# Performance work log

Hardware: AMD Instinct MI355X
Metric: run time of the kernel (lower is better)

Reference implementation:

```python
import jax, jax.numpy as jnp
import numpy as np

VOCAB = 1_000_000
EMBED_DIM = 128
BATCH = 16_384
NOISE_COUNT = 16


def setup_inputs() -> dict:
    key = jax.random.key(0)
    k1, k2, k3, k4, k5, k6 = jax.random.split(key, 6)
    embed = jax.random.uniform(k1, (EMBED_DIM, VOCAB), jnp.float32, -1.0, 1.0)
    bias = jax.random.uniform(k2, (VOCAB, 1), jnp.float32, -1.0, 1.0)
    u = jax.random.uniform(k3, (VOCAB,), jnp.float32, 1e-3, 1.0)
    freq = u / u.sum()  # normalized unigram^0.75 noise distribution
    targets = jax.random.randint(k4, (BATCH,), 0, VOCAB)
    contexts = jax.random.randint(k5, (BATCH,), 0, VOCAB)
    noises = jax.random.randint(k6, (BATCH * NOISE_COUNT,), 0, VOCAB)
    return {"embed": embed, "bias": bias, "freq": freq,
            "targets": targets, "contexts": contexts, "noises": noises,
            "noise_count": NOISE_COUNT}


def reference(embed, bias, freq, targets, contexts, noises, noise_count):
    # embed: (E, V); bias: (V, 1); freq: (V,)
    E = embed.shape[0]
    B = targets.shape[0]
    re = 10.0
    q = embed[:, targets]                      # (E, B) target embeddings
    r = embed[:, contexts]                     # (E, B) context embeddings
    b = bias[targets, 0][None, :]              # (1, B)
    s = ((r * q).sum(0)[None, :] + b) / E      # (1, B) scaled score
    # positive term: log(sigmoid(s - log(k * p(target))))
    pos = jax.nn.log_sigmoid(s - jnp.log(noise_count * freq[targets]))
    loss = pos.sum()
    # noise term: log(1 - sigmoid(tile(s,k) - log(k * p(noise)))) = log_sigmoid(-x)
    s_tiled = jnp.tile(s, (1, noise_count))    # (1, B*k) == torch.cat((s,)*k, dim=1)
    noise_loss = jax.nn.log_sigmoid(-(s_tiled - jnp.log(noise_count * freq[noises]))).sum()
    total_loss = -(loss + noise_loss) / B
    penalty = re * ((q * q).sum() + (r * r).sum()) / (E * B)
    return total_loss + penalty
```

## Files before the change

kernel.cpp:

```cpp
#include <hip/hip_runtime.h>
#include <math.h>


#define NB 2048

__device__ __forceinline__ float log_sigmoid_f(float x) {
    return fminf(x, 0.0f) - log1pf(expf(-fabsf(x)));
}

__device__ __forceinline__ int task_col(int i, const int* __restrict__ targets,
                                        const int* __restrict__ contexts) {
    const int pair = i >> 1;
    return (i & 1) ? contexts[pair] : targets[pair];
}

__global__ __launch_bounds__(256) void hist_kernel(
    const int* __restrict__ targets, const int* __restrict__ contexts,
    int* __restrict__ counts, int T2, int sh)
{
    const int i = blockIdx.x * 256 + threadIdx.x;
    if (i < T2) atomicAdd(&counts[task_col(i, targets, contexts) >> sh], 1);
}

__global__ __launch_bounds__(1024) void scan_kernel(
    const int* __restrict__ counts, int* __restrict__ cursors, int nb)
{
    __shared__ int a[NB], b[NB];
    for (int i = threadIdx.x; i < NB; i += 1024) a[i] = (i < nb) ? counts[i] : 0;
    __syncthreads();
    int* src = a; int* dst = b;
    for (int off = 1; off < NB; off <<= 1) {
        for (int i = threadIdx.x; i < NB; i += 1024)
            dst[i] = src[i] + (i >= off ? src[i - off] : 0);
        __syncthreads();
        int* t = src; src = dst; dst = t;
    }
    for (int i = threadIdx.x; i < NB; i += 1024)
        if (i < nb) cursors[i] = src[i] - counts[i];
}

__global__ __launch_bounds__(256) void scatter_kernel(
    const int* __restrict__ targets, const int* __restrict__ contexts,
    int* __restrict__ cursors, int* __restrict__ sorted,
    int* __restrict__ invperm, int T2, int sh)
{
    const int i = blockIdx.x * 256 + threadIdx.x;
    if (i < T2) {
        const int col = task_col(i, targets, contexts);
        const int pos = atomicAdd(&cursors[col >> sh], 1);
        sorted[pos] = i;
        invperm[i]  = pos;
    }
}

__global__ __launch_bounds__(256) void gather_kernel(
    const float* __restrict__ embed,
    const int* __restrict__ targets, const int* __restrict__ contexts,
    const int* __restrict__ sorted, float* __restrict__ dense,
    int V, int T2)
{
    const int p = threadIdx.x & 15;
    const int g = threadIdx.x >> 4;
    const int pos = blockIdx.x * 16 + p;
    if (pos >= T2) return;
    const int col = task_col(sorted[pos], targets, contexts);
    const int e0 = g * 8;
    const float* src = embed + col;
    float v[8];
    #pragma unroll
    for (int k = 0; k < 8; ++k) v[k] = src[(size_t)(e0 + k) * V];
    float4* dst = (float4*)(dense + (size_t)pos * 128 + e0);
    dst[0] = make_float4(v[0], v[1], v[2], v[3]);
    dst[1] = make_float4(v[4], v[5], v[6], v[7]);
}

__global__ __launch_bounds__(256) void compute_kernel(
    const float* __restrict__ dense, const int* __restrict__ invperm,
    const float* __restrict__ bias, const float* __restrict__ freq,
    const int* __restrict__ targets, const int* __restrict__ noises,
    float* __restrict__ partials, int B, int NC)
{
    __shared__ float sh_dot[16][17];
    __shared__ float sh_sq [16][17];
    __shared__ float sh_s  [16];
    __shared__ float sh_wred[4];

    const int p = threadIdx.x & 15;
    const int g = threadIdx.x >> 4;
    const int j = blockIdx.x * 16 + p;
    const bool valid = (j < B);

    float contrib = 0.0f;
    float dot = 0.0f, sq = 0.0f;
    float lg0 = 0.0f; bool has0 = false;
    float bval = 0.0f, lgt = 0.0f;

    if (valid) {
        if (g < NC) {
            const int n = noises[j + (size_t)g * B];
            lg0 = logf((float)NC * freq[n]);
            has0 = true;
        }
        if (g == 0) {
            const int t = targets[j];
            bval = bias[t];
            lgt  = logf((float)NC * freq[t]);
        }
        const int e0 = g * 8;
        const float4* qv = (const float4*)(dense + (size_t)invperm[2 * j]     * 128 + e0);
        const float4* rv = (const float4*)(dense + (size_t)invperm[2 * j + 1] * 128 + e0);
        const float4 q0 = qv[0], q1 = qv[1];
        const float4 r0 = rv[0], r1 = rv[1];
        dot = fmaf(q0.x, r0.x, fmaf(q0.y, r0.y, fmaf(q0.z, r0.z, fmaf(q0.w, r0.w,
              fmaf(q1.x, r1.x, fmaf(q1.y, r1.y, fmaf(q1.z, r1.z, q1.w * r1.w)))))));
        sq  = fmaf(q0.x, q0.x, fmaf(q0.y, q0.y, fmaf(q0.z, q0.z, fmaf(q0.w, q0.w,
              fmaf(q1.x, q1.x, fmaf(q1.y, q1.y, fmaf(q1.z, q1.z, fmaf(q1.w, q1.w,
              fmaf(r0.x, r0.x, fmaf(r0.y, r0.y, fmaf(r0.z, r0.z, fmaf(r0.w, r0.w,
              fmaf(r1.x, r1.x, fmaf(r1.y, r1.y, fmaf(r1.z, r1.z, r1.w * r1.w)))))))))))))));
    }
    sh_dot[p][g] = dot;
    sh_sq [p][g] = sq;
    __syncthreads();

    if (threadIdx.x < 16) {
        float d = 0.0f, s2 = 0.0f;
        #pragma unroll
        for (int gg = 0; gg < 16; ++gg) {
            d  += sh_dot[threadIdx.x][gg];
            s2 += sh_sq [threadIdx.x][gg];
        }
        float sval = 0.0f;
        if (valid) {
            sval = (d + bval) / 128.0f;
            const float pos = log_sigmoid_f(sval - lgt);
            contrib += -pos / (float)B + 10.0f * s2 / (128.0f * (float)B);
        }
        sh_s[threadIdx.x] = sval;
    }
    __syncthreads();

    if (valid) {
        const float sval = sh_s[p];
        float nacc = 0.0f;
        if (has0) nacc = log_sigmoid_f(-(sval - lg0));
        for (int k = g + 16; k < NC; k += 16) {
            const int n = noises[j + (size_t)k * B];
            nacc += log_sigmoid_f(-(sval - logf((float)NC * freq[n])));
        }
        contrib += -nacc / (float)B;
    }

    #pragma unroll
    for (int off = 32; off > 0; off >>= 1)
        contrib += __shfl_xor(contrib, off, 64);
    const int wave = threadIdx.x >> 6;
    if ((threadIdx.x & 63) == 0) sh_wred[wave] = contrib;
    __syncthreads();
    if (threadIdx.x == 0)
        partials[blockIdx.x] = sh_wred[0] + sh_wred[1] + sh_wred[2] + sh_wred[3];
}

__global__ __launch_bounds__(256) void reduce_partials_kernel(
    const float* __restrict__ parts, int n, float* __restrict__ out)
{
    __shared__ double sh[256];
    double a = 0.0;
    for (int i = threadIdx.x; i < n; i += 256) a += (double)parts[i];
    sh[threadIdx.x] = a;
    __syncthreads();
    for (int s = 128; s > 0; s >>= 1) {
        if (threadIdx.x < s) sh[threadIdx.x] += sh[threadIdx.x + s];
        __syncthreads();
    }
    if (threadIdx.x == 0) out[0] = (float)sh[0];
}

__global__ __launch_bounds__(256) void nce_fallback(
    const float* __restrict__ embed, const float* __restrict__ bias,
    const float* __restrict__ freq, const int* __restrict__ targets,
    const int* __restrict__ contexts, const int* __restrict__ noises,
    float* __restrict__ block_partials, int V, int E, int B, int NC)
{
    __shared__ float sh_dot[16][17];
    __shared__ float sh_sq [16][17];
    __shared__ float sh_s  [16];
    __shared__ float sh_wred[4];
    const int p = threadIdx.x & 15;
    const int g = threadIdx.x >> 4;
    const int j = blockIdx.x * 16 + p;
    const bool valid = (j < B);
    float contrib = 0.0f, dot = 0.0f, sq = 0.0f;
    float lg0 = 0.0f; bool has0 = false; float bval = 0.0f, lgt = 0.0f;
    if (valid) {
        const int t = targets[j], c = contexts[j];
        if (g < NC) { const int n = noises[j + (size_t)g * B];
                      lg0 = logf((float)NC * freq[n]); has0 = true; }
        if (g == 0) { bval = bias[t]; lgt = logf((float)NC * freq[t]); }
        const int epc = E / 16, e0 = g * epc;
        const float* ct = embed + t; const float* cc = embed + c;
        #pragma unroll 8
        for (int e = e0; e < e0 + epc; ++e) {
            float qe = ct[(size_t)e * V], re = cc[(size_t)e * V];
            dot = fmaf(qe, re, dot);
            sq  = fmaf(qe, qe, fmaf(re, re, sq));
        }
    }
    sh_dot[p][g] = dot; sh_sq[p][g] = sq;
    __syncthreads();
    if (threadIdx.x < 16) {
        float d = 0.0f, s2 = 0.0f;
        #pragma unroll
        for (int gg = 0; gg < 16; ++gg) { d += sh_dot[threadIdx.x][gg]; s2 += sh_sq[threadIdx.x][gg]; }
        float sval = 0.0f;
        if (valid) {
            sval = (d + bval) / (float)E;
            contrib += -log_sigmoid_f(sval - lgt) / (float)B + 10.0f * s2 / ((float)E * (float)B);
        }
        sh_s[threadIdx.x] = sval;
    }
    __syncthreads();
    if (valid) {
        const float sval = sh_s[p];
        float nacc = 0.0f;
        if (has0) nacc = log_sigmoid_f(-(sval - lg0));
        for (int k = g + 16; k < NC; k += 16) {
            const int n = noises[j + (size_t)k * B];
            nacc += log_sigmoid_f(-(sval - logf((float)NC * freq[n])));
        }
        contrib += -nacc / (float)B;
    }
    #pragma unroll
    for (int off = 32; off > 0; off >>= 1) contrib += __shfl_xor(contrib, off, 64);
    if ((threadIdx.x & 63) == 0) sh_wred[threadIdx.x >> 6] = contrib;
    __syncthreads();
    if (threadIdx.x == 0)
        block_partials[blockIdx.x] = sh_wred[0] + sh_wred[1] + sh_wred[2] + sh_wred[3];
}

extern "C" void kernel_launch(void* const* d_in, const int* in_sizes, int n_in,
                              void* d_out, int out_size, void* d_ws, size_t ws_size,
                              hipStream_t stream) {
    const float* embed    = (const float*)d_in[0];
    const float* bias     = (const float*)d_in[1];
    const float* freq     = (const float*)d_in[2];
    const int*   targets  = (const int*)d_in[3];
    const int*   contexts = (const int*)d_in[4];
    const int*   noises   = (const int*)d_in[5];

    const int V  = in_sizes[2];
    const int E  = in_sizes[0] / V;
    const int B  = in_sizes[3];
    const int NC = in_sizes[5] / B;
    const int T2 = 2 * B;

    char* ws = (char*)d_ws;
    float* partials = (float*)ws;
    int*   counts   = (int*)(ws + 16384);
    int*   cursors  = (int*)(ws + 16384 + NB * 4);
    int*   sorted   = (int*)(ws + 16384 + 2 * NB * 4);
    int*   invperm  = sorted + T2;
    size_t dense_off = 16384 + 2 * (size_t)NB * 4 + 2 * (size_t)T2 * 4;
    dense_off = (dense_off + 255) & ~(size_t)255;
    float* dense = (float*)(ws + dense_off);
    const size_t needed = dense_off + (size_t)T2 * 128 * 4;

    const int nblocks = (B + 15) / 16;

    if (E == 128 && (B & 15) == 0 && ws_size >= needed) {
        int sh = 0;
        while ((((V - 1) >> sh) + 1) > NB) ++sh;
        const int nb = ((V - 1) >> sh) + 1;

        hipMemsetAsync(counts, 0, (size_t)NB * 4, stream);
        hist_kernel<<<(T2 + 255) / 256, 256, 0, stream>>>(targets, contexts, counts, T2, sh);
        scan_kernel<<<1, 1024, 0, stream>>>(counts, cursors, nb);
        scatter_kernel<<<(T2 + 255) / 256, 256, 0, stream>>>(targets, contexts, cursors,
                                                             sorted, invperm, T2, sh);
        gather_kernel<<<(T2 + 15) / 16, 256, 0, stream>>>(embed, targets, contexts,
                                                          sorted, dense, V, T2);
        compute_kernel<<<nblocks, 256, 0, stream>>>(dense, invperm, bias, freq,
                                                    targets, noises, partials, B, NC);
    } else {
        nce_fallback<<<nblocks, 256, 0, stream>>>(embed, bias, freq, targets, contexts,
                                                  noises, partials, V, E, B, NC);
    }
    reduce_partials_kernel<<<1, 256, 0, stream>>>(partials, nblocks, (float*)d_out);
}
```

Before: 102.7 us.

## Store gathered embeddings as bf16 and use a wave-shuffle scan

The gathered dense embedding buffer is stored as packed bf16x8 instead of fp32, halving the intermediate write and read traffic between gather and compute. The gather thread mapping is swapped so each thread writes one 16-byte bf16 chunk contiguously. The single-block scan is rewritten from a shared-memory Hillis-Steele loop to per-thread serial sums plus a wave shuffle scan, cutting barriers. The bf16 rounding slightly changes the dot products and penalty, risking accuracy tolerance.

```diff
diff --git a/kernel.cpp b/kernel.cpp
--- a/kernel.cpp
+++ b/kernel.cpp
@@ -1,8 +1,11 @@
 #include <hip/hip_runtime.h>
+#include <hip/hip_bf16.h>
 #include <math.h>
 
 
 #define NB 2048
+
+struct alignas(16) bf16x8 { __hip_bfloat16 h[8]; };
 
 __device__ __forceinline__ float log_sigmoid_f(float x) {
     return fminf(x, 0.0f) - log1pf(expf(-fabsf(x)));
@@ -22,21 +25,39 @@
     if (i < T2) atomicAdd(&counts[task_col(i, targets, contexts) >> sh], 1);
 }
 
-__global__ __launch_bounds__(1024) void scan_kernel(
+__global__ __launch_bounds__(256) void scan_kernel(
     const int* __restrict__ counts, int* __restrict__ cursors, int nb)
 {
-    __shared__ int a[NB], b[NB];
-    for (int i = threadIdx.x; i < NB; i += 1024) a[i] = (i < nb) ? counts[i] : 0;
-    __syncthreads();
-    int* src = a; int* dst = b;
-    for (int off = 1; off < NB; off <<= 1) {
-        for (int i = threadIdx.x; i < NB; i += 1024)
-            dst[i] = src[i] + (i >= off ? src[i - off] : 0);
-        __syncthreads();
-        int* t = src; src = dst; dst = t;
-    }
-    for (int i = threadIdx.x; i < NB; i += 1024)
-        if (i < nb) cursors[i] = src[i] - counts[i];
+    __shared__ int wv_tot[4];
+    const int tid  = threadIdx.x;
+    const int lane = tid & 63;
+    const int w    = tid >> 6;
+    int v[8];
+    const int base = tid * 8;
+    int local = 0;
+    #pragma unroll
+    for (int k = 0; k < 8; ++k) {
+        const int idx = base + k;
+        v[k] = (idx < nb) ? counts[idx] : 0;
+        local += v[k];
+    }
+    int incl = local;
+    #pragma unroll
+    for (int off = 1; off < 64; off <<= 1) {
+        const int n = __shfl_up(incl, off, 64);
+        if (lane >= off) incl += n;
+    }
+    if (lane == 63) wv_tot[w] = incl;
+    __syncthreads();
+    int wpre = 0;
+    for (int i = 0; i < w; ++i) wpre += wv_tot[i];
+    int run = wpre + incl - local;
+    #pragma unroll
+    for (int k = 0; k < 8; ++k) {
+        const int idx = base + k;
+        if (idx < nb) cursors[idx] = run;
+        run += v[k];
+    }
 }
 
 __global__ __launch_bounds__(256) void scatter_kernel(
@@ -56,26 +77,26 @@
 __global__ __launch_bounds__(256) void gather_kernel(
     const float* __restrict__ embed,
     const int* __restrict__ targets, const int* __restrict__ contexts,
-    const int* __restrict__ sorted, float* __restrict__ dense,
+    const int* __restrict__ sorted, bf16x8* __restrict__ dense,
     int V, int T2)
 {
-    const int p = threadIdx.x & 15;
-    const int g = threadIdx.x >> 4;
+    const int g = threadIdx.x & 15;
+    const int p = threadIdx.x >> 4;
     const int pos = blockIdx.x * 16 + p;
     if (pos >= T2) return;
     const int col = task_col(sorted[pos], targets, contexts);
-    const int e0 = g * 8;
-    const float* src = embed + col;
+    const float* src = embed + col + (size_t)(g * 8) * V;
     float v[8];
     #pragma unroll
-    for (int k = 0; k < 8; ++k) v[k] = src[(size_t)(e0 + k) * V];
-    float4* dst = (float4*)(dense + (size_t)pos * 128 + e0);
-    dst[0] = make_float4(v[0], v[1], v[2], v[3]);
-    dst[1] = make_float4(v[4], v[5], v[6], v[7]);
+    for (int k = 0; k < 8; ++k) v[k] = src[(size_t)k * V];
+    bf16x8 outv;
+    #pragma unroll
+    for (int k = 0; k < 8; ++k) outv.h[k] = __float2bfloat16(v[k]);
+    dense[(size_t)pos * 16 + g] = outv;
 }
 
 __global__ __launch_bounds__(256) void compute_kernel(
-    const float* __restrict__ dense, const int* __restrict__ invperm,
+    const bf16x8* __restrict__ dense, const int* __restrict__ invperm,
     const float* __restrict__ bias, const float* __restrict__ freq,
     const int* __restrict__ targets, const int* __restrict__ noises,
     float* __restrict__ partials, int B, int NC)
@@ -106,17 +127,15 @@
             bval = bias[t];
             lgt  = logf((float)NC * freq[t]);
         }
-        const int e0 = g * 8;
-        const float4* qv = (const float4*)(dense + (size_t)invperm[2 * j]     * 128 + e0);
-        const float4* rv = (const float4*)(dense + (size_t)invperm[2 * j + 1] * 128 + e0);
-        const float4 q0 = qv[0], q1 = qv[1];
-        const float4 r0 = rv[0], r1 = rv[1];
-        dot = fmaf(q0.x, r0.x, fmaf(q0.y, r0.y, fmaf(q0.z, r0.z, fmaf(q0.w, r0.w,
-              fmaf(q1.x, r1.x, fmaf(q1.y, r1.y, fmaf(q1.z, r1.z, q1.w * r1.w)))))));
-        sq  = fmaf(q0.x, q0.x, fmaf(q0.y, q0.y, fmaf(q0.z, q0.z, fmaf(q0.w, q0.w,
-              fmaf(q1.x, q1.x, fmaf(q1.y, q1.y, fmaf(q1.z, q1.z, fmaf(q1.w, q1.w,
-              fmaf(r0.x, r0.x, fmaf(r0.y, r0.y, fmaf(r0.z, r0.z, fmaf(r0.w, r0.w,
-              fmaf(r1.x, r1.x, fmaf(r1.y, r1.y, fmaf(r1.z, r1.z, r1.w * r1.w)))))))))))))));
+        const bf16x8 qv = dense[(size_t)invperm[2 * j]     * 16 + g];
+        const bf16x8 rv = dense[(size_t)invperm[2 * j + 1] * 16 + g];
+        #pragma unroll
+        for (int k = 0; k < 8; ++k) {
+            const float qe = __bfloat162float(qv.h[k]);
+            const float re = __bfloat162float(rv.h[k]);
+            dot = fmaf(qe, re, dot);
+            sq  = fmaf(qe, qe, fmaf(re, re, sq));
+        }
     }
     sh_dot[p][g] = dot;
     sh_sq [p][g] = sq;
@@ -153,8 +172,7 @@
     #pragma unroll
     for (int off = 32; off > 0; off >>= 1)
         contrib += __shfl_xor(contrib, off, 64);
-    const int wave = threadIdx.x >> 6;
-    if ((threadIdx.x & 63) == 0) sh_wred[wave] = contrib;
+    if ((threadIdx.x & 63) == 0) sh_wred[threadIdx.x >> 6] = contrib;
     __syncthreads();
     if (threadIdx.x == 0)
         partials[blockIdx.x] = sh_wred[0] + sh_wred[1] + sh_wred[2] + sh_wred[3];
@@ -256,13 +274,13 @@
     char* ws = (char*)d_ws;
     float* partials = (float*)ws;
     int*   counts   = (int*)(ws + 16384);
-    int*   cursors  = (int*)(ws + 16384 + NB * 4);
-    int*   sorted   = (int*)(ws + 16384 + 2 * NB * 4);
+    int*   cursors  = counts + NB;
+    int*   sorted   = cursors + NB;
     int*   invperm  = sorted + T2;
     size_t dense_off = 16384 + 2 * (size_t)NB * 4 + 2 * (size_t)T2 * 4;
     dense_off = (dense_off + 255) & ~(size_t)255;
-    float* dense = (float*)(ws + dense_off);
-    const size_t needed = dense_off + (size_t)T2 * 128 * 4;
+    bf16x8* dense = (bf16x8*)(ws + dense_off);
+    const size_t needed = dense_off + (size_t)T2 * 128 * 2;
 
     const int nblocks = (B + 15) / 16;
 
@@ -273,7 +291,7 @@
 
         hipMemsetAsync(counts, 0, (size_t)NB * 4, stream);
         hist_kernel<<<(T2 + 255) / 256, 256, 0, stream>>>(targets, contexts, counts, T2, sh);
-        scan_kernel<<<1, 1024, 0, stream>>>(counts, cursors, nb);
+        scan_kernel<<<1, 256, 0, stream>>>(counts, cursors, nb);
         scatter_kernel<<<(T2 + 255) / 256, 256, 0, stream>>>(targets, contexts, cursors,
                                                              sorted, invperm, T2, sh);
         gather_kernel<<<(T2 + 15) / 16, 256, 0, stream>>>(embed, targets, contexts,
```

New measurement: 102.2 us. About the same (-0.5%).
